# Kernel optimization log

Hardware: AMD Instinct MI355X
Metric: run time of the kernel (lower is better)

Reference implementation:

```python
import jax, jax.numpy as jnp
import numpy as np

BETA, GAMMA = 1.0, 0.25

def _mlp(x, w1, b1, w2, b2):
    # Linear -> GELU (exact, matches torch nn.GELU default) -> Linear
    h = jax.nn.gelu(x @ w1 + b1, approximate=False)
    return h @ w2 + b2

def _mse(a, b):
    return jnp.mean(jnp.square(a - b))

def setup_inputs() -> dict:
    key = jax.random.key(0)
    ks = jax.random.split(key, 12)
    N, D_IN, D_H, D_Z = 65536, 1024, 512, 256
    CB_SIZES = [1024, 512, 256]
    def lin(k, fan_in, fan_out):
        s = 1.0 / np.sqrt(fan_in)
        kw, kb = jax.random.split(k)
        return (jax.random.uniform(kw, (fan_in, fan_out), jnp.float32, -s, s),
                jax.random.uniform(kb, (fan_out,), jnp.float32, -s, s))
    enc_w1, enc_b1 = lin(ks[0], D_IN, D_H)
    enc_w2, enc_b2 = lin(ks[1], D_H, D_Z)
    dec_w1, dec_b1 = lin(ks[2], D_Z, D_H)
    dec_w2, dec_b2 = lin(ks[3], D_H, D_IN)
    cb0 = jax.random.normal(ks[4], (CB_SIZES[0], D_Z), jnp.float32)
    cb1 = jax.random.normal(ks[5], (CB_SIZES[1], D_Z), jnp.float32)
    cb2 = jax.random.normal(ks[6], (CB_SIZES[2], D_Z), jnp.float32)
    x = jax.random.normal(ks[7], (N, D_IN), jnp.float32)
    return {"x": x,
            "enc_w1": enc_w1, "enc_b1": enc_b1, "enc_w2": enc_w2, "enc_b2": enc_b2,
            "dec_w1": dec_w1, "dec_b1": dec_b1, "dec_w2": dec_w2, "dec_b2": dec_b2,
            "cb0": cb0, "cb1": cb1, "cb2": cb2}

def _nearest(res, C):
    # argmin of squared L2 distance == argmin of cdist(p=2); indices under stop_gradient
    res_sg = jax.lax.stop_gradient(res)
    C_sg = jax.lax.stop_gradient(C)
    d2 = (jnp.sum(res_sg * res_sg, -1, keepdims=True)
          - 2.0 * (res_sg @ C_sg.T)
          + jnp.sum(C_sg * C_sg, -1))  # [N, K]
    return jnp.argmin(d2, axis=-1)

def _rq_forward(z, codebooks):
    residual = z
    output = jnp.zeros_like(z)
    losses = []
    for C in codebooks:
        idx = _nearest(residual, C)
        q = C[idx]  # embedding gather, grads flow to C
        loss = (BETA * _mse(jax.lax.stop_gradient(residual), q)
                + GAMMA * _mse(residual, jax.lax.stop_gradient(q)))
        losses.append(loss)
        output = output + q
        residual = residual - q
    return output, losses

def reference(x, enc_w1, enc_b1, enc_w2, enc_b2,
              dec_w1, dec_b1, dec_w2, dec_b2, cb0, cb1, cb2):
    z = _mlp(x, enc_w1, enc_b1, enc_w2, enc_b2)
    zq, commit = _rq_forward(z, [cb0, cb1, cb2])
    # z + zq.detach() - z.detach(): straight-through
    dec_in = z + jax.lax.stop_gradient(zq - z)
    out = _mlp(dec_in, dec_w1, dec_b1, dec_w2, dec_b2)
    recon_loss = _mse(out, x)
    return (recon_loss, commit[0], commit[1], commit[2])
```

## Files before the change

kernel.cpp:

```cpp
#include <hip/hip_runtime.h>
#include <hip/hip_bf16.h>

typedef __hip_bfloat16 bf16;
typedef __attribute__((ext_vector_type(8))) short bf16x8;
typedef __attribute__((ext_vector_type(4))) float f32x4;

#define NR 65536
#define DIN 1024
#define DH 512
#define DZ 256

__device__ __forceinline__ short f2b(float f) {
    union { __hip_bfloat16 h; short s; } u;
    u.h = __float2bfloat16(f);
    return u.s;
}
__device__ __forceinline__ float b2f(short s) {
    union { short s; __hip_bfloat16 h; } u;
    u.s = s;
    return __bfloat162float(u.h);
}

__device__ __forceinline__ void gll16(const void* g, void* l) {
    __builtin_amdgcn_global_load_lds(
        (const __attribute__((address_space(1))) char*)g,
        (__attribute__((address_space(3))) char*)l, 16, 0, 0);
}


__global__ void k_zero(double* __restrict__ p) {
    if (threadIdx.x < 4) p[threadIdx.x] = 0.0;
}

__global__ __launch_bounds__(256)
void k_prep_x(const float* __restrict__ x, bf16* __restrict__ xb) {
    const size_t stride = (size_t)gridDim.x * 256 * 8;
    for (size_t i = ((size_t)blockIdx.x * 256 + threadIdx.x) * 8;
         i < (size_t)NR * DIN; i += stride) {
        f32x4 a = *(const f32x4*)(x + i);
        f32x4 b = *(const f32x4*)(x + i + 4);
        bf16x8 o;
        o[0]=f2b(a[0]); o[1]=f2b(a[1]); o[2]=f2b(a[2]); o[3]=f2b(a[3]);
        o[4]=f2b(b[0]); o[5]=f2b(b[1]); o[6]=f2b(b[2]); o[7]=f2b(b[3]);
        *(bf16x8*)((short*)xb + i) = o;
    }
}

__global__ __launch_bounds__(256)
void k_wt(const float* __restrict__ w, bf16* __restrict__ wT, int K, int N) {
    __shared__ float t[64][65];
    const int k0 = blockIdx.x * 64, n0 = blockIdx.y * 64;
    const int tx = threadIdx.x & 63, ty = threadIdx.x >> 6;
    #pragma unroll
    for (int i = 0; i < 16; i++) {
        int r = ty + i * 4;
        t[r][tx] = w[(size_t)(k0 + r) * N + n0 + tx];
    }
    __syncthreads();
    #pragma unroll
    for (int i = 0; i < 16; i++) {
        int r = ty + i * 4;
        wT[(size_t)(n0 + r) * K + k0 + tx] = __float2bfloat16(t[tx][r]);
    }
}

__global__ void k_cb(const float* __restrict__ cb, bf16* __restrict__ cbb,
                     float* __restrict__ cnorm) {
    int cw = blockIdx.x, d = threadIdx.x;
    int dsrc = d ^ ((cw & 7) << 3);
    float v = cb[(size_t)cw * DZ + dsrc];
    cbb[(size_t)cw * DZ + d] = __float2bfloat16(v);
    float s = v * v;
    #pragma unroll
    for (int m = 1; m < 64; m <<= 1) s += __shfl_xor(s, m, 64);
    __shared__ float red[4];
    if ((d & 63) == 0) red[d >> 6] = s;
    __syncthreads();
    if (d == 0) cnorm[cw] = red[0] + red[1] + red[2] + red[3];
}


template <int EPI, int LOGG>
__global__ __launch_bounds__(256)
void k_gemm(const bf16* __restrict__ A, const bf16* __restrict__ BT,
            const float* __restrict__ bias, bf16* __restrict__ outb,
            const bf16* __restrict__ xref, double* __restrict__ lossAcc,
            int M, int N, int K) {
    __shared__ __align__(16) char AsBuf[8192];
    __shared__ __align__(16) char BsBuf[8192];
    const int tid = threadIdx.x;
    const int bid = blockIdx.x;
    const int tt = bid >> 3;
    const int bn = tt & ((1 << LOGG) - 1);
    const int bm = (bid & 7) + ((tt >> LOGG) << 3);
    const int w = tid >> 6, l = tid & 63, g = l >> 4, c = l & 15;
    const int wr = w >> 1, wc = w & 1;

    f32x4 acc[4][4] = {};

    const int o1 = tid * 16;
    const int o2 = o1 + 4096;
    const int br1 = o1 >> 6, bcol1 = (o1 & 63) >> 1;
    const int br2 = o2 >> 6, bcol2 = (o2 & 63) >> 1;
    const bf16* Abase = A + (size_t)(bm * 128) * K;
    const bf16* Bbase = BT + (size_t)(bn * 128) * K;

    for (int k0 = 0; k0 < K; k0 += 32) {
        __syncthreads();
        gll16(Abase + (size_t)br1 * K + k0 + bcol1, AsBuf + o1);
        gll16(Abase + (size_t)br2 * K + k0 + bcol2, AsBuf + o2);
        gll16(Bbase + (size_t)br1 * K + k0 + bcol1, BsBuf + o1);
        gll16(Bbase + (size_t)br2 * K + k0 + bcol2, BsBuf + o2);
        __syncthreads();

        bf16x8 af[4], bfr[4];
        #pragma unroll
        for (int m = 0; m < 4; m++)
            af[m] = *(const bf16x8*)((const bf16*)AsBuf + (wr * 64 + m * 16 + c) * 32 + g * 8);
        #pragma unroll
        for (int n = 0; n < 4; n++)
            bfr[n] = *(const bf16x8*)((const bf16*)BsBuf + (wc * 64 + n * 16 + c) * 32 + g * 8);
        #pragma unroll
        for (int m = 0; m < 4; m++)
            #pragma unroll
            for (int n = 0; n < 4; n++)
                acc[m][n] = __builtin_amdgcn_mfma_f32_16x16x32_bf16(
                    af[m], bfr[n], acc[m][n], 0, 0, 0);
    }

    float msum = 0.f;
    #pragma unroll
    for (int n = 0; n < 4; n++) {
        const int col = bn * 128 + wc * 64 + n * 16 + c;
        const float bv = bias[col];
        #pragma unroll
        for (int m = 0; m < 4; m++) {
            const int row0 = bm * 128 + wr * 64 + m * 16 + g * 4;
            #pragma unroll
            for (int r = 0; r < 4; r++) {
                float v = acc[m][n][r] + bv;
                int row = row0 + r;
                if (EPI == 0) {
                    float ge = 0.5f * v * (1.f + erff(v * 0.70710678118654752f));
                    outb[(size_t)row * N + col] = __float2bfloat16(ge);
                } else if (EPI == 1) {
                    outb[(size_t)row * N + col] = __float2bfloat16(v);
                } else {
                    float d = v - __bfloat162float(xref[(size_t)row * N + col]);
                    msum += d * d;
                }
            }
        }
    }
    if (EPI == 2) {
        #pragma unroll
        for (int m = 1; m < 64; m <<= 1) msum += __shfl_xor(msum, m, 64);
        if (l == 0) atomicAdd(lossAcc, (double)msum);
    }
}


__global__ __launch_bounds__(256)
void k_rq(const bf16* __restrict__ z, const bf16* __restrict__ cbb,
          const float* __restrict__ cnorm,
          const float* __restrict__ cbf0, const float* __restrict__ cbf1,
          const float* __restrict__ cbf2,
          bf16* __restrict__ zqb, double* __restrict__ lossAcc) {
    __shared__ __align__(16) char mt[65536];
    __shared__ float cn_lds[1792];
    const int tid = threadIdx.x;
    const int w = tid >> 6, l = tid & 63, g = l >> 4, c = l & 15;
    const int rowbase = blockIdx.x * 128 + w * 32;

    for (int i = tid; i < 1792; i += 256) cn_lds[i] = cnorm[i];

    bf16x8 af[2][8];
    #pragma unroll
    for (int m = 0; m < 2; m++) {
        const short* zp = (const short*)z + (size_t)(rowbase + m * 16 + c) * DZ + g * 8;
        #pragma unroll
        for (int kk = 0; kk < 8; kk++)
            af[m][kk] = *(const bf16x8*)(zp + kk * 32);
    }

    const int c0 = c & 7;
    const int Pbase = c * 512 + ((g * 16) ^ ((c0 & 3) << 4)) + ((c0 >> 2) << 6);

    const float* cbf[3] = {cbf0, cbf1, cbf2};
    const int Ks[3] = {1024, 512, 256};
    int mtg = 0, cnbase = 0;
    float lsum[3];

    for (int s = 0; s < 3; s++) {
        const int nmt = Ks[s] >> 7;
        float minv[2][4] = {{3.4e38f, 3.4e38f, 3.4e38f, 3.4e38f},
                            {3.4e38f, 3.4e38f, 3.4e38f, 3.4e38f}};
        int mini[2][4] = {};
        for (int imt = 0; imt < nmt; imt++, mtg++) {
            __syncthreads();
            const char* src = (const char*)cbb + (size_t)mtg * 65536 + tid * 16;
            #pragma unroll
            for (int st = 0; st < 16; st++)
                gll16(src + (size_t)st * 4096, mt + st * 4096 + tid * 16);
            __syncthreads();
            #pragma unroll
            for (int sub = 0; sub < 8; sub++) {
                const char* tp = mt + sub * 8192;
                bf16x8 bfr[8];
                #pragma unroll
                for (int kk = 0; kk < 8; kk++)
                    bfr[kk] = *(const bf16x8*)(tp + (Pbase ^ (kk << 6)));
                f32x4 a0 = {0.f, 0.f, 0.f, 0.f}, a1 = {0.f, 0.f, 0.f, 0.f};
                #pragma unroll
                for (int kk = 0; kk < 8; kk++) {
                    a0 = __builtin_amdgcn_mfma_f32_16x16x32_bf16(af[0][kk], bfr[kk], a0, 0, 0, 0);
                    a1 = __builtin_amdgcn_mfma_f32_16x16x32_bf16(af[1][kk], bfr[kk], a1, 0, 0, 0);
                }
                const int cw = imt * 128 + sub * 16 + c;
                const float cn = cn_lds[cnbase + cw];
                #pragma unroll
                for (int r = 0; r < 4; r++) {
                    float d0 = cn - 2.0f * a0[r];
                    if (d0 < minv[0][r]) { minv[0][r] = d0; mini[0][r] = cw; }
                    float d1 = cn - 2.0f * a1[r];
                    if (d1 < minv[1][r]) { minv[1][r] = d1; mini[1][r] = cw; }
                }
            }
        }
        float ls = 0.f;
        #pragma unroll
        for (int m = 0; m < 2; m++) {
            #pragma unroll
            for (int mm = 1; mm < 16; mm <<= 1) {
                #pragma unroll
                for (int r = 0; r < 4; r++) {
                    float ov = __shfl_xor(minv[m][r], mm, 64);
                    int   oi = __shfl_xor(mini[m][r], mm, 64);
                    if (ov < minv[m][r] || (ov == minv[m][r] && oi < mini[m][r])) {
                        minv[m][r] = ov; mini[m][r] = oi;
                    }
                }
            }
            int srcl = (c >> 2) << 4;
            int i0 = __shfl(mini[m][0], srcl, 64);
            int i1 = __shfl(mini[m][1], srcl, 64);
            int i2 = __shfl(mini[m][2], srcl, 64);
            int i3 = __shfl(mini[m][3], srcl, 64);
            int rr = c & 3;
            int myidx = rr == 0 ? i0 : rr == 1 ? i1 : rr == 2 ? i2 : i3;

            const float* qp = cbf[s] + (size_t)myidx * DZ + g * 8;
            #pragma unroll
            for (int kk = 0; kk < 8; kk++) {
                f32x4 q0 = *(const f32x4*)(qp + kk * 32);
                f32x4 q1 = *(const f32x4*)(qp + kk * 32 + 4);
                bf16x8 a = af[m][kk];
                bf16x8 t;
                #pragma unroll
                for (int j = 0; j < 4; j++) {
                    float d = b2f(a[j]) - q0[j];
                    ls += d * d; t[j] = f2b(d);
                }
                #pragma unroll
                for (int j = 0; j < 4; j++) {
                    float d = b2f(a[4 + j]) - q1[j];
                    ls += d * d; t[4 + j] = f2b(d);
                }
                af[m][kk] = t;
            }
        }
        lsum[s] = ls;
        cnbase += Ks[s];
    }

    #pragma unroll
    for (int m = 0; m < 2; m++) {
        const short* zp = (const short*)z + (size_t)(rowbase + m * 16 + c) * DZ + g * 8;
        short* op = (short*)zqb + (size_t)(rowbase + m * 16 + c) * DZ + g * 8;
        #pragma unroll
        for (int kk = 0; kk < 8; kk++) {
            bf16x8 zv = *(const bf16x8*)(zp + kk * 32);
            bf16x8 a = af[m][kk];
            bf16x8 o;
            #pragma unroll
            for (int j = 0; j < 8; j++)
                o[j] = f2b(b2f(zv[j]) - b2f(a[j]));
            *(bf16x8*)(op + kk * 32) = o;
        }
    }

    #pragma unroll
    for (int s = 0; s < 3; s++) {
        float v = lsum[s];
        #pragma unroll
        for (int mm = 1; mm < 64; mm <<= 1) v += __shfl_xor(v, mm, 64);
        if (l == 0) atomicAdd(&lossAcc[1 + s], (double)v);
    }
}


__global__ void k_fin(const double* __restrict__ la, float* __restrict__ out) {
    int i = threadIdx.x;
    if (i == 0) out[0] = (float)(la[0] / ((double)NR * DIN));
    if (i == 1) out[1] = (float)(1.25 * la[1] / ((double)NR * DZ));
    if (i == 2) out[2] = (float)(1.25 * la[2] / ((double)NR * DZ));
    if (i == 3) out[3] = (float)(1.25 * la[3] / ((double)NR * DZ));
}


extern "C" void kernel_launch(void* const* d_in, const int* in_sizes, int n_in,
                              void* d_out, int out_size, void* d_ws, size_t ws_size,
                              hipStream_t stream) {
    (void)in_sizes; (void)n_in; (void)out_size; (void)ws_size;
    const float* x   = (const float*)d_in[0];
    const float* ew1 = (const float*)d_in[1];
    const float* eb1 = (const float*)d_in[2];
    const float* ew2 = (const float*)d_in[3];
    const float* eb2 = (const float*)d_in[4];
    const float* dw1 = (const float*)d_in[5];
    const float* db1 = (const float*)d_in[6];
    const float* dw2 = (const float*)d_in[7];
    const float* db2 = (const float*)d_in[8];
    const float* cb0 = (const float*)d_in[9];
    const float* cb1 = (const float*)d_in[10];
    const float* cb2 = (const float*)d_in[11];

    char* ws = (char*)d_ws;
    double* lossAcc = (double*)ws;
    size_t off = 256;
    bf16* xb = (bf16*)(ws + off);
    off += (size_t)NR * DIN * 2;
    bf16* h1 = (bf16*)(ws + off);
    bf16* h2 = h1;
    off += (size_t)NR * DH * 2;
    bf16* zb = (bf16*)(ws + off);
    off += (size_t)NR * DZ * 2;
    bf16* w1T = (bf16*)(ws + off); off += (size_t)DH * DIN * 2;
    bf16* w2T = (bf16*)(ws + off); off += (size_t)DZ * DH * 2;
    bf16* w3T = (bf16*)(ws + off); off += (size_t)DH * DZ * 2;
    bf16* w4T = (bf16*)(ws + off); off += (size_t)DIN * DH * 2;
    bf16* cbb = (bf16*)(ws + off); off += (size_t)1792 * DZ * 2;
    float* cnorm = (float*)(ws + off); off += 1792 * 4;

    k_zero<<<1, 64, 0, stream>>>(lossAcc);
    k_prep_x<<<4096, 256, 0, stream>>>(x, xb);
    k_wt<<<dim3(DIN / 64, DH / 64), 256, 0, stream>>>(ew1, w1T, DIN, DH);
    k_wt<<<dim3(DH / 64, DZ / 64), 256, 0, stream>>>(ew2, w2T, DH, DZ);
    k_wt<<<dim3(DZ / 64, DH / 64), 256, 0, stream>>>(dw1, w3T, DZ, DH);
    k_wt<<<dim3(DH / 64, DIN / 64), 256, 0, stream>>>(dw2, w4T, DH, DIN);
    k_cb<<<1024, 256, 0, stream>>>(cb0, cbb, cnorm);
    k_cb<<<512, 256, 0, stream>>>(cb1, cbb + (size_t)1024 * DZ, cnorm + 1024);
    k_cb<<<256, 256, 0, stream>>>(cb2, cbb + (size_t)1536 * DZ, cnorm + 1536);

    k_gemm<0, 2><<<(DH / 128) * (NR / 128), 256, 0, stream>>>(
        xb, w1T, eb1, h1, nullptr, nullptr, NR, DH, DIN);
    k_gemm<1, 1><<<(DZ / 128) * (NR / 128), 256, 0, stream>>>(
        h1, w2T, eb2, zb, nullptr, nullptr, NR, DZ, DH);

    k_rq<<<NR / 128, 256, 0, stream>>>(zb, cbb, cnorm, cb0, cb1, cb2, zb, lossAcc);

    k_gemm<0, 2><<<(DH / 128) * (NR / 128), 256, 0, stream>>>(
        zb, w3T, db1, h2, nullptr, nullptr, NR, DH, DZ);
    k_gemm<2, 3><<<(DIN / 128) * (NR / 128), 256, 0, stream>>>(
        h2, w4T, db2, nullptr, xb, lossAcc, NR, DIN, DH);

    k_fin<<<1, 64, 0, stream>>>(lossAcc, (float*)d_out);
}
```

Before: 681.5 us.

## Double GEMM K-tile to 64 and XOR-swizzle LDS layout to avoid bank conflicts

The GEMM k-step grows from 32 to 64, so each block loads 128x64 tiles of A and B per iteration, halving the number of barrier pairs. Shared memory rows are now 128 bytes with an XOR swizzle on the 16-byte chunk index, applied both on the global-to-LDS load side and on the fragment reads, to reduce LDS bank conflicts. LDS use doubles to 32KB per block, which may lower occupancy.

```diff
diff --git a/kernel.cpp b/kernel.cpp
--- a/kernel.cpp
+++ b/kernel.cpp
@@ -86,8 +86,8 @@
             const float* __restrict__ bias, bf16* __restrict__ outb,
             const bf16* __restrict__ xref, double* __restrict__ lossAcc,
             int M, int N, int K) {
-    __shared__ __align__(16) char AsBuf[8192];
-    __shared__ __align__(16) char BsBuf[8192];
+    __shared__ __align__(16) char AsBuf[16384];
+    __shared__ __align__(16) char BsBuf[16384];
     const int tid = threadIdx.x;
     const int bid = blockIdx.x;
     const int tt = bid >> 3;
@@ -99,33 +99,46 @@
     f32x4 acc[4][4] = {};
 
     const int o1 = tid * 16;
-    const int o2 = o1 + 4096;
-    const int br1 = o1 >> 6, bcol1 = (o1 & 63) >> 1;
-    const int br2 = o2 >> 6, bcol2 = (o2 & 63) >> 1;
+    int srow[4], scol[4];
+    #pragma unroll
+    for (int j = 0; j < 4; j++) {
+        const int ob = o1 + j * 4096;
+        srow[j] = ob >> 7;
+        scol[j] = (((ob & 127) >> 4) ^ (srow[j] & 7)) << 3;
+    }
     const bf16* Abase = A + (size_t)(bm * 128) * K;
     const bf16* Bbase = BT + (size_t)(bn * 128) * K;
 
-    for (int k0 = 0; k0 < K; k0 += 32) {
+    for (int k0 = 0; k0 < K; k0 += 64) {
         __syncthreads();
-        gll16(Abase + (size_t)br1 * K + k0 + bcol1, AsBuf + o1);
-        gll16(Abase + (size_t)br2 * K + k0 + bcol2, AsBuf + o2);
-        gll16(Bbase + (size_t)br1 * K + k0 + bcol1, BsBuf + o1);
-        gll16(Bbase + (size_t)br2 * K + k0 + bcol2, BsBuf + o2);
+        #pragma unroll
+        for (int j = 0; j < 4; j++)
+            gll16(Abase + (size_t)srow[j] * K + k0 + scol[j], AsBuf + o1 + j * 4096);
+        #pragma unroll
+        for (int j = 0; j < 4; j++)
+            gll16(Bbase + (size_t)srow[j] * K + k0 + scol[j], BsBuf + o1 + j * 4096);
         __syncthreads();
 
-        bf16x8 af[4], bfr[4];
-        #pragma unroll
-        for (int m = 0; m < 4; m++)
-            af[m] = *(const bf16x8*)((const bf16*)AsBuf + (wr * 64 + m * 16 + c) * 32 + g * 8);
-        #pragma unroll
-        for (int n = 0; n < 4; n++)
-            bfr[n] = *(const bf16x8*)((const bf16*)BsBuf + (wc * 64 + n * 16 + c) * 32 + g * 8);
-        #pragma unroll
-        for (int m = 0; m < 4; m++)
-            #pragma unroll
-            for (int n = 0; n < 4; n++)
-                acc[m][n] = __builtin_amdgcn_mfma_f32_16x16x32_bf16(
-                    af[m], bfr[n], acc[m][n], 0, 0, 0);
+        #pragma unroll
+        for (int h = 0; h < 2; h++) {
+            bf16x8 af[4], bfr[4];
+            #pragma unroll
+            for (int m = 0; m < 4; m++) {
+                const int rr = wr * 64 + m * 16 + c;
+                af[m] = *(const bf16x8*)(AsBuf + rr * 128 + (((h << 2) + g) ^ (rr & 7)) * 16);
+            }
+            #pragma unroll
+            for (int n = 0; n < 4; n++) {
+                const int rr = wc * 64 + n * 16 + c;
+                bfr[n] = *(const bf16x8*)(BsBuf + rr * 128 + (((h << 2) + g) ^ (rr & 7)) * 16);
+            }
+            #pragma unroll
+            for (int m = 0; m < 4; m++)
+                #pragma unroll
+                for (int n = 0; n < 4; n++)
+                    acc[m][n] = __builtin_amdgcn_mfma_f32_16x16x32_bf16(
+                        af[m], bfr[n], acc[m][n], 0, 0, 0);
+        }
     }
 
     float msum = 0.f;
```

New measurement: 677.3 us. Within noise of the previous version (-0.6%).
